# Kernel optimization log

Measured on AMD Instinct MI355X. Metric: run time of the kernel, lower is better.

## Reference

```python
import jax, jax.numpy as jnp
import numpy as np

N, E, H, C, L = 10000, 320000, 4, 128, 4  # nodes, edges, heads, hidden, gat layers
D_IN, E_DIM = 7, 5


def setup_inputs() -> dict:
    key = jax.random.key(0)
    ks = jax.random.split(key, 16)
    g = lambda i, shape, s=0.05: jax.random.normal(ks[i], shape, dtype=jnp.float32) * s
    z = lambda *s: jnp.zeros(s, jnp.float32)
    o = lambda *s: jnp.ones(s, jnp.float32)
    return {
        "x": g(0, (N, D_IN), 1.0),
        "edge_index": jax.random.randint(ks[1], (2, E), 0, N),
        "edge_attr": g(2, (E, E_DIM), 1.0),
        "emb_W": g(3, (D_IN, C)), "emb_b": z(C),
        "gat_Wl": g(4, (L, C, H * C)), "gat_Wr": g(5, (L, C, H * C)),
        "gat_We": g(6, (L, E_DIM, H * C)), "gat_att": g(7, (L, H, C)),
        "gat_b": z(L, C), "ln_g": o(L, C), "ln_b": z(L, C),
        "sp_W1": g(8, (2 * C, C)), "sp_b1": z(C),
        "sp_W2": g(9, (C, C)), "sp_b2": z(C),
        "sp_gW": g(10, (C, C)), "sp_gb": z(C),
        "fn_g": o(C), "fn_b": z(C),
    }


def _layernorm(x, g, b, eps=1e-5):
    m = x.mean(-1, keepdims=True)
    v = ((x - m) ** 2).mean(-1, keepdims=True)
    return (x - m) * jax.lax.rsqrt(v + eps) * g + b


def _gatv2(h, src, dst, edge_attr, Wl, Wr, We, att, b):
    # GATv2Conv(concat=False, edge_dim): x_j = Wl h[src], x_i = Wr h[dst]
    xl = (h @ Wl).reshape(-1, H, C)            # [N,H,C]
    xr = (h @ Wr).reshape(-1, H, C)            # [N,H,C]
    e = (edge_attr @ We).reshape(-1, H, C)      # [E,H,C]
    m = jax.nn.leaky_relu(xl[src] + xr[dst] + e, 0.2)
    logits = jnp.einsum('ehc,hc->eh', m, att)   # [E,H]
    mx = jax.ops.segment_max(logits, dst, num_segments=N)
    ex = jnp.exp(logits - mx[dst])
    den = jax.ops.segment_sum(ex, dst, num_segments=N)
    alpha = ex / den[dst]                       # softmax over incoming edges
    out = jax.ops.segment_sum(alpha[..., None] * xl[src], dst, num_segments=N)
    return out.mean(axis=1) + b                 # head-average (concat=False)


def _social_pool(h, src, dst, W1, b1, W2, b2, gW, gb):
    pair = jnp.concatenate([h[src], h[dst]], axis=-1)   # [E,2C]
    inter = jax.nn.relu(pair @ W1 + b1) @ W2 + b2       # [E,C]
    gated = inter * jax.nn.sigmoid(inter @ gW + gb)
    s = jax.ops.segment_sum(gated, src, num_segments=N)
    cnt = jax.ops.segment_sum(jnp.ones((src.shape[0],), h.dtype), src, num_segments=N)
    return s / jnp.maximum(cnt, 1.0)[:, None]           # scatter-mean


def reference(x, edge_index, edge_attr, emb_W, emb_b, gat_Wl, gat_Wr, gat_We,
              gat_att, gat_b, ln_g, ln_b, sp_W1, sp_b1, sp_W2, sp_b2,
              sp_gW, sp_gb, fn_g, fn_b):
    src, dst = edge_index[0], edge_index[1]
    h = jax.nn.relu(x @ emb_W + emb_b)
    for i in range(L):
        res = h
        h = _gatv2(h, src, dst, edge_attr, gat_Wl[i], gat_Wr[i], gat_We[i],
                   gat_att[i], gat_b[i])
        h = jax.nn.relu(h)
        h = _layernorm(h + res, ln_g[i], ln_b[i])
    h = h + _social_pool(h, src, dst, sp_W1, sp_b1, sp_W2, sp_b2, sp_gW, sp_gb)
    return _layernorm(h, fn_g, fn_b)
```

## Files before the change

kernel.cpp:

```cpp
#include <hip/hip_runtime.h>
#include <hip/hip_bf16.h>
#include <math.h>

#define N_NODES 10000
#define N_EDGES 320000
#define HEADS   4
#define CDIM    128
#define HC      512
#define LAYERS  4
#define DIN     7
#define EDIM    5

typedef short short8 __attribute__((ext_vector_type(8)));
typedef unsigned short us8 __attribute__((ext_vector_type(8)));
typedef float f32x4 __attribute__((ext_vector_type(4)));

__device__ __forceinline__ void atomAddF(float* p, float v) { unsafeAtomicAdd(p, v); }

__device__ __forceinline__ unsigned short f2bf(float f) {
  unsigned u = __float_as_uint(f);
  unsigned r = u + 0x7fffu + ((u >> 16) & 1u);
  return (unsigned short)(r >> 16);
}
__device__ __forceinline__ float bf2f(unsigned short u) {
  return __uint_as_float(((unsigned)u) << 16);
}

__global__ __launch_bounds__(256) void embed_kernel(
    const float* __restrict__ x, const float* __restrict__ W,
    const float* __restrict__ b, float* __restrict__ h, unsigned short* __restrict__ hbf)
{
  int t = blockIdx.x * 256 + threadIdx.x;
  int n = t >> 7, c = t & 127;
  float acc = b[c];
#pragma unroll
  for (int k = 0; k < DIN; ++k) acc += x[n * DIN + k] * W[k * CDIM + c];
  acc = fmaxf(acc, 0.f);
  h[t] = acc;
  hbf[t] = f2bf(acc);
}

__global__ __launch_bounds__(256) void pack_kernel(
    const float* __restrict__ Wl, const float* __restrict__ Wr,
    const float* __restrict__ W1, const float* __restrict__ W2,
    const float* __restrict__ gW, unsigned short* __restrict__ WlrT,
    unsigned short* __restrict__ W1T, unsigned short* __restrict__ W2T,
    unsigned short* __restrict__ gWT, unsigned short* __restrict__ W2bf)
{
  int t = blockIdx.x * 256 + threadIdx.x;
  if (t < 524288) {
    int k = t & 127, n = (t >> 7) & 1023, l = t >> 17;
    float v = (n < 512) ? Wl[(size_t)(l * 128 + k) * 512 + n]
                        : Wr[(size_t)(l * 128 + k) * 512 + (n - 512)];
    WlrT[t] = f2bf(v);
  } else if (t < 524288 + 32768) {
    int u = t - 524288; int k = u & 127, n = u >> 7;
    float v = (n < 128) ? W1[k * 128 + n] : W1[(128 + k) * 128 + (n - 128)];
    W1T[u] = f2bf(v);
  } else if (t < 557056 + 16384) {
    int u = t - 557056; int k = u & 127, n = u >> 7;
    W2T[u] = f2bf(W2[k * 128 + n]);
  } else if (t < 573440 + 16384) {
    int u = t - 573440; int k = u & 127, n = u >> 7;
    gWT[u] = f2bf(gW[k * 128 + n]);
  } else if (t < 589824 + 16384) {
    int u = t - 589824;
    W2bf[u] = f2bf(W2[u]);
  }
}

__global__ __launch_bounds__(128) void fuse_bias_kernel(
    const float* __restrict__ b2, const float* __restrict__ gW,
    const float* __restrict__ gb, float* __restrict__ gbF)
{
  int n = threadIdx.x;
  float s = gb[n];
  for (int k = 0; k < 128; ++k) s += b2[k] * gW[k * 128 + n];
  gbF[n] = s;
}

__global__ __launch_bounds__(256) void hist_kernel(
    const int* __restrict__ ei, int* __restrict__ degD, int* __restrict__ degS)
{
  int e = blockIdx.x * 256 + threadIdx.x;
  if (e < N_EDGES) {
    atomicAdd(&degS[ei[e]], 1);
    atomicAdd(&degD[ei[N_EDGES + e]], 1);
  }
}

__global__ __launch_bounds__(1024) void scan_kernel(
    const int* __restrict__ degD, int* __restrict__ offD, int* __restrict__ curD,
    const int* __restrict__ degS, int* __restrict__ offS, int* __restrict__ curS, int n)
{
  __shared__ int wsum[16];
  __shared__ int carry;
  int tid = threadIdx.x, wid = tid >> 6, lane = tid & 63;
  for (int arr = 0; arr < 2; ++arr) {
    const int* deg = arr ? degS : degD;
    int* off = arr ? offS : offD;
    int* cur = arr ? curS : curD;
    if (tid == 0) carry = 0;
    __syncthreads();
    for (int base = 0; base < n; base += 1024) {
      int i = base + tid;
      int v = (i < n) ? deg[i] : 0;
      int incl = v;
#pragma unroll
      for (int o = 1; o < 64; o <<= 1) {
        int t2 = __shfl_up(incl, o);
        if (lane >= o) incl += t2;
      }
      if (lane == 63) wsum[wid] = incl;
      __syncthreads();
      if (tid < 16) {
        int wv = wsum[tid];
#pragma unroll
        for (int o = 1; o < 16; o <<= 1) {
          int t2 = __shfl_up(wv, o);
          if (tid >= o) wv += t2;
        }
        wsum[tid] = wv;
      }
      __syncthreads();
      int woff = (wid > 0) ? wsum[wid - 1] : 0;
      int excl = carry + woff + incl - v;
      if (i < n) { off[i] = excl; cur[i] = excl; }
      __syncthreads();
      if (tid == 0) carry += wsum[15];
      __syncthreads();
    }
    if (tid == 0) off[n] = carry;
    __syncthreads();
  }
}

__global__ __launch_bounds__(256) void scatter_kernel(
    const int* __restrict__ ei, int* __restrict__ curD, int* __restrict__ curS,
    int* __restrict__ eidD, int* __restrict__ eidS)
{
  int e = blockIdx.x * 256 + threadIdx.x;
  if (e < N_EDGES) {
    int s = ei[e], d = ei[N_EDGES + e];
    int p = atomicAdd(&curD[d], 1);
    eidD[p] = e;
    int q = atomicAdd(&curS[s], 1);
    eidS[q] = e;
  }
}

__global__ __launch_bounds__(256) void reorder_kernel(
    const int* __restrict__ ei, const float* __restrict__ eattr,
    const int* __restrict__ eidD, int* __restrict__ esrc,
    float4* __restrict__ ea4, float* __restrict__ ea1)
{
  int idx = blockIdx.x * 256 + threadIdx.x;
  if (idx < N_EDGES) {
    int e = eidD[idx];
    esrc[idx] = ei[e];
    const float* p = &eattr[(size_t)e * 5];
    ea4[idx] = make_float4(p[0], p[1], p[2], p[3]);
    ea1[idx] = p[4];
  }
}

__global__ __launch_bounds__(256) void mfma_gemm_kernel(
    const unsigned short* __restrict__ A, const unsigned short* __restrict__ BT,
    unsigned short* __restrict__ C, int M, int ldc)
{
  __shared__ __align__(16) unsigned short sA[64 * 128];
  __shared__ __align__(16) unsigned short sB[64 * 128];
  int tid = threadIdx.x;
  int bm = blockIdx.y * 64, bn = blockIdx.x * 64;
#pragma unroll
  for (int i = 0; i < 4; ++i) {
    int ch = tid + i * 256;
    int r = ch >> 4, kc = ch & 15;
    int gr = bm + r;
    short8 v = {0, 0, 0, 0, 0, 0, 0, 0};
    if (gr < M) v = *(const short8*)&A[(size_t)gr * 128 + kc * 8];
    *(short8*)&sA[r * 128 + ((kc ^ (r & 7)) * 8)] = v;
  }
#pragma unroll
  for (int i = 0; i < 4; ++i) {
    int ch = tid + i * 256;
    int r = ch >> 4, kc = ch & 15;
    short8 v = *(const short8*)&BT[(size_t)(bn + r) * 128 + kc * 8];
    *(short8*)&sB[r * 128 + ((kc ^ (r & 7)) * 8)] = v;
  }
  __syncthreads();
  int w = tid >> 6, lane = tid & 63;
  int wr = (w >> 1) * 32, wc = (w & 1) * 32;
  int l15 = lane & 15, q = lane >> 4;
  f32x4 acc00 = {0, 0, 0, 0}, acc01 = acc00, acc10 = acc00, acc11 = acc00;
#pragma unroll
  for (int ks = 0; ks < 4; ++ks) {
    int c0 = ks * 4 + q;
    int m0 = wr + l15, m1 = m0 + 16;
    int n0 = wc + l15, n1 = n0 + 16;
    short8 a0 = *(const short8*)&sA[m0 * 128 + ((c0 ^ (m0 & 7)) * 8)];
    short8 a1 = *(const short8*)&sA[m1 * 128 + ((c0 ^ (m1 & 7)) * 8)];
    short8 b0 = *(const short8*)&sB[n0 * 128 + ((c0 ^ (n0 & 7)) * 8)];
    short8 b1 = *(const short8*)&sB[n1 * 128 + ((c0 ^ (n1 & 7)) * 8)];
    acc00 = __builtin_amdgcn_mfma_f32_16x16x32_bf16(a0, b0, acc00, 0, 0, 0);
    acc01 = __builtin_amdgcn_mfma_f32_16x16x32_bf16(a0, b1, acc01, 0, 0, 0);
    acc10 = __builtin_amdgcn_mfma_f32_16x16x32_bf16(a1, b0, acc10, 0, 0, 0);
    acc11 = __builtin_amdgcn_mfma_f32_16x16x32_bf16(a1, b1, acc11, 0, 0, 0);
  }
#pragma unroll
  for (int mf = 0; mf < 2; ++mf) {
#pragma unroll
    for (int nf = 0; nf < 2; ++nf) {
      f32x4 acc = mf == 0 ? (nf == 0 ? acc00 : acc01) : (nf == 0 ? acc10 : acc11);
      int col = bn + wc + nf * 16 + l15;
#pragma unroll
      for (int r = 0; r < 4; ++r) {
        int row = bm + wr + mf * 16 + 4 * q + r;
        if (row < M) C[(size_t)row * ldc + col] = f2bf(acc[r]);
      }
    }
  }
}

__global__ __launch_bounds__(256) void gat_agg_kernel(
    const float* __restrict__ h_in, float* __restrict__ h_out,
    unsigned short* __restrict__ hbf_out, const unsigned short* __restrict__ xlr,
    const int* __restrict__ esrc, const float4* __restrict__ ea4,
    const float* __restrict__ ea1, const int* __restrict__ offD,
    const float* __restrict__ We, const float* __restrict__ att,
    const float* __restrict__ gbias, const float* __restrict__ lng,
    const float* __restrict__ lnb)
{
  int tid = threadIdx.x;
  int w = tid >> 6, lane = tid & 63;
  int n = blockIdx.x * 4 + w;
  int base = lane * 8;

  float wWe[5][8];
#pragma unroll
  for (int k = 0; k < 5; ++k) {
    float4 a = *(const float4*)&We[k * HC + base];
    float4 b = *(const float4*)&We[k * HC + base + 4];
    wWe[k][0] = a.x; wWe[k][1] = a.y; wWe[k][2] = a.z; wWe[k][3] = a.w;
    wWe[k][4] = b.x; wWe[k][5] = b.y; wWe[k][6] = b.z; wWe[k][7] = b.w;
  }
  float wAtt[8];
  {
    float4 a = *(const float4*)&att[base];
    float4 b = *(const float4*)&att[base + 4];
    wAtt[0] = a.x; wAtt[1] = a.y; wAtt[2] = a.z; wAtt[3] = a.w;
    wAtt[4] = b.x; wAtt[5] = b.y; wAtt[6] = b.z; wAtt[7] = b.w;
  }
  float xr_reg[8];
  {
    us8 u = *(const us8*)&xlr[(size_t)n * 1024 + 512 + base];
#pragma unroll
    for (int j = 0; j < 8; ++j) xr_reg[j] = bf2f(u[j]);
  }

  int e0 = offD[n], e1 = offD[n + 1];
  float m = -INFINITY, dsum = 0.f;
  float acc[8] = {0.f, 0.f, 0.f, 0.f, 0.f, 0.f, 0.f, 0.f};

  us8 uA = {0, 0, 0, 0, 0, 0, 0, 0}, uB = uA;
  float4 qaA = {0, 0, 0, 0}, qaB = {0, 0, 0, 0};
  float qeA = 0.f, qeB = 0.f;
  int sA1 = 0, sB1 = 0;

  if (e0 < e1) {
    int iB = (e0 + 1 < e1) ? e0 + 1 : e0;
    int sA0 = esrc[e0], sB0 = esrc[iB];
    uA = *(const us8*)&xlr[(size_t)sA0 * 1024 + base];
    uB = *(const us8*)&xlr[(size_t)sB0 * 1024 + base];
    qaA = ea4[e0]; qeA = ea1[e0];
    qaB = ea4[iB]; qeB = ea1[iB];
    int jA = (e0 + 2 < e1) ? e0 + 2 : e0;
    int jB = (e0 + 3 < e1) ? e0 + 3 : e0;
    sA1 = esrc[jA]; sB1 = esrc[jB];
  }

  for (int i = e0; i < e1; i += 2) {
    float x0[8], x1[8];
#pragma unroll
    for (int j = 0; j < 8; ++j) { x0[j] = bf2f(uA[j]); x1[j] = bf2f(uB[j]); }
    float a0 = qaA.x, a1 = qaA.y, a2 = qaA.z, a3 = qaA.w, a4 = qeA;
    float b0 = qaB.x, b1 = qaB.y, b2 = qaB.z, b3 = qaB.w, b4 = qeB;

    uA = *(const us8*)&xlr[(size_t)sA1 * 1024 + base];
    uB = *(const us8*)&xlr[(size_t)sB1 * 1024 + base];
    {
      int jA = (i + 2 < e1) ? i + 2 : e0;
      int jB = (i + 3 < e1) ? i + 3 : e0;
      qaA = ea4[jA]; qeA = ea1[jA];
      qaB = ea4[jB]; qeB = ea1[jB];
      int kA = (i + 4 < e1) ? i + 4 : e0;
      int kB = (i + 5 < e1) ? i + 5 : e0;
      sA1 = esrc[kA]; sB1 = esrc[kB];
    }

    float lg0 = 0.f, lg1 = 0.f;
#pragma unroll
    for (int j = 0; j < 8; ++j) {
      float v0 = x0[j] + xr_reg[j] + a0 * wWe[0][j] + a1 * wWe[1][j]
               + a2 * wWe[2][j] + a3 * wWe[3][j] + a4 * wWe[4][j];
      v0 = (v0 > 0.f) ? v0 : 0.2f * v0;
      lg0 += v0 * wAtt[j];
      float v1 = x1[j] + xr_reg[j] + b0 * wWe[0][j] + b1 * wWe[1][j]
               + b2 * wWe[2][j] + b3 * wWe[3][j] + b4 * wWe[4][j];
      v1 = (v1 > 0.f) ? v1 : 0.2f * v1;
      lg1 += v1 * wAtt[j];
    }
    lg0 += __shfl_xor(lg0, 1); lg1 += __shfl_xor(lg1, 1);
    lg0 += __shfl_xor(lg0, 2); lg1 += __shfl_xor(lg1, 2);
    lg0 += __shfl_xor(lg0, 4); lg1 += __shfl_xor(lg1, 4);
    lg0 += __shfl_xor(lg0, 8); lg1 += __shfl_xor(lg1, 8);
    lg1 = (i + 1 < e1) ? lg1 : -INFINITY;

    float nm = fmaxf(m, fmaxf(lg0, lg1));
    float sc = __expf(m - nm);
    float p0 = __expf(lg0 - nm);
    float p1 = __expf(lg1 - nm);
    dsum = dsum * sc + p0 + p1;
#pragma unroll
    for (int j = 0; j < 8; ++j) acc[j] = (acc[j] * sc + p0 * x0[j]) + p1 * x1[j];
    m = nm;
  }

  float inv = (dsum > 0.f) ? (1.f / dsum) : 0.f;
  int c8 = (lane & 15) * 8;
  float o[8];
  float s1 = 0.f, s2 = 0.f;
#pragma unroll
  for (int j = 0; j < 8; ++j) {
    float v = acc[j] * inv;
    v += __shfl_xor(v, 16);
    v += __shfl_xor(v, 32);
    float oo = 0.25f * v + gbias[c8 + j];
    oo = fmaxf(oo, 0.f);
    oo += h_in[(size_t)n * 128 + c8 + j];
    o[j] = oo;
    s1 += oo; s2 += oo * oo;
  }
  s1 += __shfl_xor(s1, 1);  s2 += __shfl_xor(s2, 1);
  s1 += __shfl_xor(s1, 2);  s2 += __shfl_xor(s2, 2);
  s1 += __shfl_xor(s1, 4);  s2 += __shfl_xor(s2, 4);
  s1 += __shfl_xor(s1, 8);  s2 += __shfl_xor(s2, 8);
  s1 += __shfl_xor(s1, 16); s2 += __shfl_xor(s2, 16);
  s1 += __shfl_xor(s1, 32); s2 += __shfl_xor(s2, 32);
  float mean = s1 * (1.f / 512.f);
  float var = s2 * (1.f / 512.f) - mean * mean;
  float rs = rsqrtf(var + 1e-5f);
  if (lane < 16) {
#pragma unroll
    for (int j = 0; j < 8; ++j) {
      float val = (o[j] - mean) * rs * lng[c8 + j] + lnb[c8 + j];
      h_out[(size_t)n * 128 + c8 + j] = val;
      hbf_out[(size_t)n * 128 + c8 + j] = f2bf(val);
    }
  }
}

__global__ __launch_bounds__(512) void sp_edge_kernel(
    const unsigned short* __restrict__ sab, const float* __restrict__ b1,
    const unsigned short* __restrict__ W2T, const float* __restrict__ b2,
    const unsigned short* __restrict__ FT, const float* __restrict__ gbF,
    const int* __restrict__ ei, const int* __restrict__ eidS,
    float* __restrict__ pool)
{
  __shared__ __align__(16) unsigned short sT[64 * 128];
  __shared__ int rsrc[64];
  __shared__ int rdst[64];
  int tid = threadIdx.x;
  int w = tid >> 6, lane = tid & 63;
  int l15 = lane & 15, q = lane >> 4;
  int col = w * 16 + l15;

  short8 bW[4], bF[4];
#pragma unroll
  for (int ks = 0; ks < 4; ++ks) {
    bW[ks] = *(const short8*)&W2T[(size_t)col * 128 + (ks * 4 + q) * 8];
    bF[ks] = *(const short8*)&FT [(size_t)col * 128 + (ks * 4 + q) * 8];
  }
  float b2c = b2[col];
  float gbc = gbF[col];

  int ebase = blockIdx.x * 64;
  if (tid < 64) {
    int e = eidS[ebase + tid];
    rsrc[tid] = ei[e];
    rdst[tid] = ei[N_EDGES + e];
  }
  __syncthreads();

#pragma unroll
  for (int i = 0; i < 2; ++i) {
    int ch = tid + i * 512;
    int r = ch >> 4, kc = ch & 15, c0 = kc * 8;
    int s = rsrc[r], d = rdst[r];
    us8 ua = *(const us8*)&sab[(size_t)s * 256 + c0];
    us8 ub = *(const us8*)&sab[(size_t)d * 256 + 128 + c0];
    float4 bb0 = *(const float4*)&b1[c0];
    float4 bb1 = *(const float4*)&b1[c0 + 4];
    float bv[8] = {bb0.x, bb0.y, bb0.z, bb0.w, bb1.x, bb1.y, bb1.z, bb1.w};
    short8 o;
#pragma unroll
    for (int j = 0; j < 8; ++j)
      o[j] = (short)f2bf(fmaxf(bf2f(ua[j]) + bf2f(ub[j]) + bv[j], 0.f));
    *(short8*)&sT[r * 128 + ((kc ^ (r & 7)) * 8)] = o;
  }
  __syncthreads();

#pragma unroll
  for (int rg = 0; rg < 4; ++rg) {
    int m = rg * 16 + l15;
    f32x4 acc1 = {0, 0, 0, 0}, acc2 = {0, 0, 0, 0};
#pragma unroll
    for (int ks = 0; ks < 4; ++ks) {
      short8 a = *(const short8*)&sT[m * 128 + (((ks * 4 + q) ^ (m & 7)) * 8)];
      acc1 = __builtin_amdgcn_mfma_f32_16x16x32_bf16(a, bW[ks], acc1, 0, 0, 0);
      acc2 = __builtin_amdgcn_mfma_f32_16x16x32_bf16(a, bF[ks], acc2, 0, 0, 0);
    }
    int rb = rg * 16 + 4 * q;
    float g[4];
#pragma unroll
    for (int r = 0; r < 4; ++r) {
      float inter = acc1[r] + b2c;
      float gg = acc2[r] + gbc;
      g[r] = inter * (1.f / (1.f + __expf(-gg)));
    }
    int s0 = rsrc[rb], s1 = rsrc[rb + 1], s2 = rsrc[rb + 2], s3 = rsrc[rb + 3];
    float run = g[0]; int cur = s0;
    if (s1 == cur) run += g[1];
    else { atomAddF(&pool[(size_t)cur * 128 + col], run); cur = s1; run = g[1]; }
    if (s2 == cur) run += g[2];
    else { atomAddF(&pool[(size_t)cur * 128 + col], run); cur = s2; run = g[2]; }
    if (s3 == cur) run += g[3];
    else { atomAddF(&pool[(size_t)cur * 128 + col], run); cur = s3; run = g[3]; }
    atomAddF(&pool[(size_t)cur * 128 + col], run);
  }
}

__global__ __launch_bounds__(256) void finalize_kernel(
    const float* __restrict__ h, const float* __restrict__ pool,
    const int* __restrict__ degS, const float* __restrict__ g,
    const float* __restrict__ b, float* __restrict__ out)
{
  int t = blockIdx.x * 256 + threadIdx.x;
  int n = t >> 6, lane = t & 63;
  if (n >= N_NODES) return;
  float cnt = fmaxf((float)degS[n], 1.f);
  float a = h[(size_t)n * 128 + lane] + pool[(size_t)n * 128 + lane] / cnt;
  float c2 = h[(size_t)n * 128 + 64 + lane] + pool[(size_t)n * 128 + 64 + lane] / cnt;
  float s = a + c2, s2 = a * a + c2 * c2;
#pragma unroll
  for (int o = 1; o < 64; o <<= 1) { s += __shfl_xor(s, o); s2 += __shfl_xor(s2, o); }
  float mean = s * (1.f / 128.f);
  float var = s2 * (1.f / 128.f) - mean * mean;
  float rs = rsqrtf(var + 1e-5f);
  out[(size_t)n * 128 + lane] = (a - mean) * rs * g[lane] + b[lane];
  out[(size_t)n * 128 + 64 + lane] = (c2 - mean) * rs * g[64 + lane] + b[64 + lane];
}

extern "C" void kernel_launch(void* const* d_in, const int* in_sizes, int n_in,
                              void* d_out, int out_size, void* d_ws, size_t ws_size,
                              hipStream_t stream) {
  (void)in_sizes; (void)n_in; (void)out_size; (void)ws_size;
  const float* x     = (const float*)d_in[0];
  const int*   ei    = (const int*)d_in[1];
  const float* eattr = (const float*)d_in[2];
  const float* embW  = (const float*)d_in[3];
  const float* embB  = (const float*)d_in[4];
  const float* gWl   = (const float*)d_in[5];
  const float* gWr   = (const float*)d_in[6];
  const float* gWe   = (const float*)d_in[7];
  const float* gAtt  = (const float*)d_in[8];
  const float* gB    = (const float*)d_in[9];
  const float* lnG   = (const float*)d_in[10];
  const float* lnB   = (const float*)d_in[11];
  const float* spW1  = (const float*)d_in[12];
  const float* spB1  = (const float*)d_in[13];
  const float* spW2  = (const float*)d_in[14];
  const float* spB2  = (const float*)d_in[15];
  const float* spGW  = (const float*)d_in[16];
  const float* spGB  = (const float*)d_in[17];
  const float* fnG   = (const float*)d_in[18];
  const float* fnB   = (const float*)d_in[19];
  float* out = (float*)d_out;

  char* ws = (char*)d_ws;
  size_t off = 0;
  auto alloc = [&](size_t bytes) {
    void* p = ws + off;
    off = (off + bytes + 255) & ~(size_t)255;
    return p;
  };
  float* hA   = (float*)alloc((size_t)N_NODES * 128 * 4);
  float* hB   = (float*)alloc((size_t)N_NODES * 128 * 4);
  unsigned short* hbfA = (unsigned short*)alloc((size_t)N_NODES * 128 * 2);
  unsigned short* hbfB = (unsigned short*)alloc((size_t)N_NODES * 128 * 2);
  unsigned short* xlr  = (unsigned short*)alloc((size_t)N_NODES * 1024 * 2);
  unsigned short* sab  = (unsigned short*)alloc((size_t)N_NODES * 256 * 2);
  float* pool = (float*)alloc((size_t)N_NODES * 128 * 4);
  unsigned short* WlrT = (unsigned short*)alloc((size_t)4 * 1024 * 128 * 2);
  unsigned short* W1T  = (unsigned short*)alloc((size_t)256 * 128 * 2);
  unsigned short* W2T  = (unsigned short*)alloc((size_t)128 * 128 * 2);
  unsigned short* gWT  = (unsigned short*)alloc((size_t)128 * 128 * 2);
  unsigned short* W2bf = (unsigned short*)alloc((size_t)128 * 128 * 2);
  unsigned short* FT   = (unsigned short*)alloc((size_t)128 * 128 * 2);
  float* gbF = (float*)alloc((size_t)128 * 4);
  int* degD = (int*)alloc((size_t)N_NODES * 4);
  int* degS = (int*)alloc((size_t)N_NODES * 4);
  int* offD = (int*)alloc((size_t)(N_NODES + 1) * 4);
  int* offS = (int*)alloc((size_t)(N_NODES + 1) * 4);
  int* curD = (int*)alloc((size_t)N_NODES * 4);
  int* curS = (int*)alloc((size_t)N_NODES * 4);
  int* eidD = (int*)alloc((size_t)N_EDGES * 4);
  int* eidS = (int*)alloc((size_t)N_EDGES * 4);
  int* esrc = (int*)alloc((size_t)N_EDGES * 4);
  float4* ea4 = (float4*)alloc((size_t)N_EDGES * 16);
  float* ea1 = (float*)alloc((size_t)N_EDGES * 4);

  hipMemsetAsync(degD, 0, (size_t)N_NODES * 4, stream);
  hipMemsetAsync(degS, 0, (size_t)N_NODES * 4, stream);
  hipMemsetAsync(pool, 0, (size_t)N_NODES * 128 * 4, stream);

  pack_kernel<<<(606208 + 255) / 256, 256, 0, stream>>>(gWl, gWr, spW1, spW2, spGW,
                                                        WlrT, W1T, W2T, gWT, W2bf);
  mfma_gemm_kernel<<<dim3(2, 2), 256, 0, stream>>>(gWT, W2bf, FT, 128, 128);
  fuse_bias_kernel<<<1, 128, 0, stream>>>(spB2, spGW, spGB, gbF);

  embed_kernel<<<(N_NODES * 128) / 256, 256, 0, stream>>>(x, embW, embB, hA, hbfA);
  hist_kernel<<<(N_EDGES + 255) / 256, 256, 0, stream>>>(ei, degD, degS);
  scan_kernel<<<1, 1024, 0, stream>>>(degD, offD, curD, degS, offS, curS, N_NODES);
  scatter_kernel<<<(N_EDGES + 255) / 256, 256, 0, stream>>>(ei, curD, curS, eidD, eidS);
  reorder_kernel<<<(N_EDGES + 255) / 256, 256, 0, stream>>>(ei, eattr, eidD, esrc, ea4, ea1);

  const int MB64 = (N_NODES + 63) / 64;
  float* hcur = hA; float* hnext = hB;
  unsigned short* hbcur = hbfA; unsigned short* hbnext = hbfB;
  for (int l = 0; l < LAYERS; ++l) {
    mfma_gemm_kernel<<<dim3(16, MB64), 256, 0, stream>>>(
        hbcur, WlrT + (size_t)l * 1024 * 128, xlr, N_NODES, 1024);
    gat_agg_kernel<<<(N_NODES + 3) / 4, 256, 0, stream>>>(hcur, hnext, hbnext, xlr,
                                                          esrc, ea4, ea1, offD,
                                                          gWe + (size_t)l * EDIM * HC,
                                                          gAtt + (size_t)l * HC,
                                                          gB + (size_t)l * 128,
                                                          lnG + (size_t)l * 128,
                                                          lnB + (size_t)l * 128);
    float* t1 = hcur; hcur = hnext; hnext = t1;
    unsigned short* t2 = hbcur; hbcur = hbnext; hbnext = t2;
  }
  mfma_gemm_kernel<<<dim3(4, MB64), 256, 0, stream>>>(hbcur, W1T, sab, N_NODES, 256);
  sp_edge_kernel<<<N_EDGES / 64, 512, 0, stream>>>(sab, spB1, W2T, spB2, FT, gbF,
                                                   ei, eidS, pool);
  finalize_kernel<<<(N_NODES + 3) / 4, 256, 0, stream>>>(hcur, pool, degS, fnG, fnB, out);
}
```

Before: 757.7 us.

## Deepen GAT edge prefetch to four edges and batch social-pool atomics via LDS

The GAT aggregation loop now processes four edges per iteration with two staggered prefetch groups, giving more gather loads in flight to hide latency. Its clamp index also changes from e0 to the last edge. The social-pool edge kernel stages the gated outputs in a padded LDS buffer. It then has 256 threads walk 32 sorted rows each per column, merging runs of equal source before issuing atomics, which cuts global atomic traffic. The cost is more registers in the GAT loop, an extra sync and LDS pass, and half the threads idle in the atomic phase.

```diff
diff --git a/kernel.cpp b/kernel.cpp
--- a/kernel.cpp
+++ b/kernel.cpp
@@ -262,68 +262,107 @@
   float m = -INFINITY, dsum = 0.f;
   float acc[8] = {0.f, 0.f, 0.f, 0.f, 0.f, 0.f, 0.f, 0.f};
 
-  us8 uA = {0, 0, 0, 0, 0, 0, 0, 0}, uB = uA;
-  float4 qaA = {0, 0, 0, 0}, qaB = {0, 0, 0, 0};
-  float qeA = 0.f, qeB = 0.f;
-  int sA1 = 0, sB1 = 0;
-
   if (e0 < e1) {
-    int iB = (e0 + 1 < e1) ? e0 + 1 : e0;
-    int sA0 = esrc[e0], sB0 = esrc[iB];
-    uA = *(const us8*)&xlr[(size_t)sA0 * 1024 + base];
-    uB = *(const us8*)&xlr[(size_t)sB0 * 1024 + base];
-    qaA = ea4[e0]; qeA = ea1[e0];
-    qaB = ea4[iB]; qeB = ea1[iB];
-    int jA = (e0 + 2 < e1) ? e0 + 2 : e0;
-    int jB = (e0 + 3 < e1) ? e0 + 3 : e0;
-    sA1 = esrc[jA]; sB1 = esrc[jB];
-  }
-
-  for (int i = e0; i < e1; i += 2) {
-    float x0[8], x1[8];
-#pragma unroll
-    for (int j = 0; j < 8; ++j) { x0[j] = bf2f(uA[j]); x1[j] = bf2f(uB[j]); }
-    float a0 = qaA.x, a1 = qaA.y, a2 = qaA.z, a3 = qaA.w, a4 = qeA;
-    float b0 = qaB.x, b1 = qaB.y, b2 = qaB.z, b3 = qaB.w, b4 = qeB;
-
-    uA = *(const us8*)&xlr[(size_t)sA1 * 1024 + base];
-    uB = *(const us8*)&xlr[(size_t)sB1 * 1024 + base];
-    {
-      int jA = (i + 2 < e1) ? i + 2 : e0;
-      int jB = (i + 3 < e1) ? i + 3 : e0;
-      qaA = ea4[jA]; qeA = ea1[jA];
-      qaB = ea4[jB]; qeB = ea1[jB];
-      int kA = (i + 4 < e1) ? i + 4 : e0;
-      int kB = (i + 5 < e1) ? i + 5 : e0;
-      sA1 = esrc[kA]; sB1 = esrc[kB];
+    int last = e1 - 1;
+    int ib = (e0 + 1 < e1) ? e0 + 1 : last;
+    int ic = (e0 + 2 < e1) ? e0 + 2 : last;
+    int id2 = (e0 + 3 < e1) ? e0 + 3 : last;
+    us8 uA = *(const us8*)&xlr[(size_t)esrc[e0] * 1024 + base];
+    us8 uB = *(const us8*)&xlr[(size_t)esrc[ib] * 1024 + base];
+    us8 uC = *(const us8*)&xlr[(size_t)esrc[ic] * 1024 + base];
+    us8 uD = *(const us8*)&xlr[(size_t)esrc[id2] * 1024 + base];
+    float4 qaA = ea4[e0]; float qeA = ea1[e0];
+    float4 qaB = ea4[ib]; float qeB = ea1[ib];
+    int j4 = (e0 + 4 < e1) ? e0 + 4 : last;
+    int j5 = (e0 + 5 < e1) ? e0 + 5 : last;
+    int sN0 = esrc[j4], sN1 = esrc[j5];
+
+    for (int i = e0; i < e1; i += 4) {
+      float x0[8], x1[8];
+#pragma unroll
+      for (int j = 0; j < 8; ++j) { x0[j] = bf2f(uA[j]); x1[j] = bf2f(uB[j]); }
+      uA = *(const us8*)&xlr[(size_t)sN0 * 1024 + base];
+      uB = *(const us8*)&xlr[(size_t)sN1 * 1024 + base];
+      int j2 = (i + 2 < e1) ? i + 2 : last;
+      int j3 = (i + 3 < e1) ? i + 3 : last;
+      float4 qaC = ea4[j2]; float qeC = ea1[j2];
+      float4 qaD = ea4[j3]; float qeD = ea1[j3];
+      int j6 = (i + 6 < e1) ? i + 6 : last;
+      int j7 = (i + 7 < e1) ? i + 7 : last;
+      int sN2 = esrc[j6], sN3 = esrc[j7];
+
+      float lg0 = 0.f, lg1 = 0.f;
+#pragma unroll
+      for (int j = 0; j < 8; ++j) {
+        float v0 = x0[j] + xr_reg[j] + qaA.x * wWe[0][j] + qaA.y * wWe[1][j]
+                 + qaA.z * wWe[2][j] + qaA.w * wWe[3][j] + qeA * wWe[4][j];
+        v0 = (v0 > 0.f) ? v0 : 0.2f * v0;
+        lg0 += v0 * wAtt[j];
+        float v1 = x1[j] + xr_reg[j] + qaB.x * wWe[0][j] + qaB.y * wWe[1][j]
+                 + qaB.z * wWe[2][j] + qaB.w * wWe[3][j] + qeB * wWe[4][j];
+        v1 = (v1 > 0.f) ? v1 : 0.2f * v1;
+        lg1 += v1 * wAtt[j];
+      }
+      lg0 += __shfl_xor(lg0, 1); lg1 += __shfl_xor(lg1, 1);
+      lg0 += __shfl_xor(lg0, 2); lg1 += __shfl_xor(lg1, 2);
+      lg0 += __shfl_xor(lg0, 4); lg1 += __shfl_xor(lg1, 4);
+      lg0 += __shfl_xor(lg0, 8); lg1 += __shfl_xor(lg1, 8);
+      lg1 = (i + 1 < e1) ? lg1 : -INFINITY;
+      {
+        float nm = fmaxf(m, fmaxf(lg0, lg1));
+        float sc = __expf(m - nm);
+        float p0 = __expf(lg0 - nm);
+        float p1 = __expf(lg1 - nm);
+        dsum = dsum * sc + p0 + p1;
+#pragma unroll
+        for (int j = 0; j < 8; ++j)
+          acc[j] = fmaf(p1, x1[j], fmaf(p0, x0[j], acc[j] * sc));
+        m = nm;
+      }
+
+      float x2[8], x3[8];
+#pragma unroll
+      for (int j = 0; j < 8; ++j) { x2[j] = bf2f(uC[j]); x3[j] = bf2f(uD[j]); }
+      uC = *(const us8*)&xlr[(size_t)sN2 * 1024 + base];
+      uD = *(const us8*)&xlr[(size_t)sN3 * 1024 + base];
+      int j4b = (i + 4 < e1) ? i + 4 : last;
+      int j5b = (i + 5 < e1) ? i + 5 : last;
+      qaA = ea4[j4b]; qeA = ea1[j4b];
+      qaB = ea4[j5b]; qeB = ea1[j5b];
+      int j8 = (i + 8 < e1) ? i + 8 : last;
+      int j9 = (i + 9 < e1) ? i + 9 : last;
+      sN0 = esrc[j8]; sN1 = esrc[j9];
+
+      float lg2 = 0.f, lg3 = 0.f;
+#pragma unroll
+      for (int j = 0; j < 8; ++j) {
+        float v2 = x2[j] + xr_reg[j] + qaC.x * wWe[0][j] + qaC.y * wWe[1][j]
+                 + qaC.z * wWe[2][j] + qaC.w * wWe[3][j] + qeC * wWe[4][j];
+        v2 = (v2 > 0.f) ? v2 : 0.2f * v2;
+        lg2 += v2 * wAtt[j];
+        float v3 = x3[j] + xr_reg[j] + qaD.x * wWe[0][j] + qaD.y * wWe[1][j]
+                 + qaD.z * wWe[2][j] + qaD.w * wWe[3][j] + qeD * wWe[4][j];
+        v3 = (v3 > 0.f) ? v3 : 0.2f * v3;
+        lg3 += v3 * wAtt[j];
+      }
+      lg2 += __shfl_xor(lg2, 1); lg3 += __shfl_xor(lg3, 1);
+      lg2 += __shfl_xor(lg2, 2); lg3 += __shfl_xor(lg3, 2);
+      lg2 += __shfl_xor(lg2, 4); lg3 += __shfl_xor(lg3, 4);
+      lg2 += __shfl_xor(lg2, 8); lg3 += __shfl_xor(lg3, 8);
+      lg2 = (i + 2 < e1) ? lg2 : -INFINITY;
+      lg3 = (i + 3 < e1) ? lg3 : -INFINITY;
+      {
+        float nm = fmaxf(m, fmaxf(lg2, lg3));
+        float sc = __expf(m - nm);
+        float p2 = __expf(lg2 - nm);
+        float p3 = __expf(lg3 - nm);
+        dsum = dsum * sc + p2 + p3;
+#pragma unroll
+        for (int j = 0; j < 8; ++j)
+          acc[j] = fmaf(p3, x3[j], fmaf(p2, x2[j], acc[j] * sc));
+        m = nm;
+      }
     }
-
-    float lg0 = 0.f, lg1 = 0.f;
-#pragma unroll
-    for (int j = 0; j < 8; ++j) {
-      float v0 = x0[j] + xr_reg[j] + a0 * wWe[0][j] + a1 * wWe[1][j]
-               + a2 * wWe[2][j] + a3 * wWe[3][j] + a4 * wWe[4][j];
-      v0 = (v0 > 0.f) ? v0 : 0.2f * v0;
-      lg0 += v0 * wAtt[j];
-      float v1 = x1[j] + xr_reg[j] + b0 * wWe[0][j] + b1 * wWe[1][j]
-               + b2 * wWe[2][j] + b3 * wWe[3][j] + b4 * wWe[4][j];
-      v1 = (v1 > 0.f) ? v1 : 0.2f * v1;
-      lg1 += v1 * wAtt[j];
-    }
-    lg0 += __shfl_xor(lg0, 1); lg1 += __shfl_xor(lg1, 1);
-    lg0 += __shfl_xor(lg0, 2); lg1 += __shfl_xor(lg1, 2);
-    lg0 += __shfl_xor(lg0, 4); lg1 += __shfl_xor(lg1, 4);
-    lg0 += __shfl_xor(lg0, 8); lg1 += __shfl_xor(lg1, 8);
-    lg1 = (i + 1 < e1) ? lg1 : -INFINITY;
-
-    float nm = fmaxf(m, fmaxf(lg0, lg1));
-    float sc = __expf(m - nm);
-    float p0 = __expf(lg0 - nm);
-    float p1 = __expf(lg1 - nm);
-    dsum = dsum * sc + p0 + p1;
-#pragma unroll
-    for (int j = 0; j < 8; ++j) acc[j] = (acc[j] * sc + p0 * x0[j]) + p1 * x1[j];
-    m = nm;
   }
 
   float inv = (dsum > 0.f) ? (1.f / dsum) : 0.f;
@@ -367,9 +406,10 @@
     const int* __restrict__ ei, const int* __restrict__ eidS,
     float* __restrict__ pool)
 {
-  __shared__ __align__(16) unsigned short sT[64 * 128];
+  __shared__ __align__(16) float gT[128 * 65];
   __shared__ int rsrc[64];
   __shared__ int rdst[64];
+  unsigned short* sT = (unsigned short*)gT;
   int tid = threadIdx.x;
   int w = tid >> 6, lane = tid & 63;
   int l15 = lane & 15, q = lane >> 4;
@@ -410,33 +450,46 @@
   }
   __syncthreads();
 
+  f32x4 acc1[4], acc2[4];
 #pragma unroll
   for (int rg = 0; rg < 4; ++rg) {
-    int m = rg * 16 + l15;
-    f32x4 acc1 = {0, 0, 0, 0}, acc2 = {0, 0, 0, 0};
+    int mr = rg * 16 + l15;
+    acc1[rg] = (f32x4){0, 0, 0, 0};
+    acc2[rg] = (f32x4){0, 0, 0, 0};
 #pragma unroll
     for (int ks = 0; ks < 4; ++ks) {
-      short8 a = *(const short8*)&sT[m * 128 + (((ks * 4 + q) ^ (m & 7)) * 8)];
-      acc1 = __builtin_amdgcn_mfma_f32_16x16x32_bf16(a, bW[ks], acc1, 0, 0, 0);
-      acc2 = __builtin_amdgcn_mfma_f32_16x16x32_bf16(a, bF[ks], acc2, 0, 0, 0);
+      short8 a = *(const short8*)&sT[mr * 128 + (((ks * 4 + q) ^ (mr & 7)) * 8)];
+      acc1[rg] = __builtin_amdgcn_mfma_f32_16x16x32_bf16(a, bW[ks], acc1[rg], 0, 0, 0);
+      acc2[rg] = __builtin_amdgcn_mfma_f32_16x16x32_bf16(a, bF[ks], acc2[rg], 0, 0, 0);
     }
+  }
+  __syncthreads();
+
+#pragma unroll
+  for (int rg = 0; rg < 4; ++rg) {
     int rb = rg * 16 + 4 * q;
-    float g[4];
 #pragma unroll
     for (int r = 0; r < 4; ++r) {
-      float inter = acc1[r] + b2c;
-      float gg = acc2[r] + gbc;
-      g[r] = inter * (1.f / (1.f + __expf(-gg)));
+      float inter = acc1[rg][r] + b2c;
+      float gg = acc2[rg][r] + gbc;
+      gT[col * 65 + rb + r] = inter * (1.f / (1.f + __expf(-gg)));
     }
-    int s0 = rsrc[rb], s1 = rsrc[rb + 1], s2 = rsrc[rb + 2], s3 = rsrc[rb + 3];
-    float run = g[0]; int cur = s0;
-    if (s1 == cur) run += g[1];
-    else { atomAddF(&pool[(size_t)cur * 128 + col], run); cur = s1; run = g[1]; }
-    if (s2 == cur) run += g[2];
-    else { atomAddF(&pool[(size_t)cur * 128 + col], run); cur = s2; run = g[2]; }
-    if (s3 == cur) run += g[3];
-    else { atomAddF(&pool[(size_t)cur * 128 + col], run); cur = s3; run = g[3]; }
-    atomAddF(&pool[(size_t)cur * 128 + col], run);
+  }
+  __syncthreads();
+
+  if (tid < 256) {
+    int c = tid & 127, half = tid >> 7;
+    int rbeg = half * 32, rend = rbeg + 32;
+    int curs = -1; float run = 0.f;
+    for (int r = rbeg; r < rend; ++r) {
+      int s = rsrc[r];
+      if (s != curs) {
+        if (curs >= 0) atomAddF(&pool[(size_t)curs * 128 + c], run);
+        curs = s; run = 0.f;
+      }
+      run += gT[c * 65 + r];
+    }
+    atomAddF(&pool[(size_t)curs * 128 + c], run);
   }
 }
 
```

Result: faster. 721.2 us (-4.8%).
